# Performance work log

Measured on AMD Instinct MI355X. Metric: run time of the kernel, lower is better.

## Reference

```python
import jax, jax.numpy as jnp
import numpy as np

DT = 1.0  # LEM base time-step


def _conv(x, w, b):
    # x: [B,C,H,W], w: [O,I,kh,kw] 'SAME' stride-1 conv (kernel=3, padding=1)
    y = jax.lax.conv_general_dilated(
        x, w, window_strides=(1, 1), padding='SAME',
        dimension_numbers=('NCHW', 'OIHW', 'NCHW'))
    return y + b[None, :, None, None]


def setup_inputs() -> dict:
    key = jax.random.key(0)
    ks = jax.random.split(key, 7)
    B, Cin, Cout, T, H, W, K = 8, 32, 32, 50, 64, 64, 3
    s = 0.1
    return {
        'X':  jax.random.normal(ks[0], (B, Cin, T, H, W), jnp.float32),
        'Wx': jax.random.normal(ks[1], (4 * Cout, Cin, K, K), jnp.float32) * s,
        'bx': jnp.zeros((4 * Cout,), jnp.float32),
        'Wy': jax.random.normal(ks[2], (3 * Cout, Cout, K, K), jnp.float32) * s,
        'by': jnp.zeros((3 * Cout,), jnp.float32),
        'Wz': jax.random.normal(ks[3], (Cout, Cout, K, K), jnp.float32) * s,
        'bz': jnp.zeros((Cout,), jnp.float32),
    }


def reference(X, Wx, bx, Wy, by, Wz, bz):
    B, Cin, T, H, W = X.shape
    Cout = Wz.shape[0]

    def step(carry, x_t):
        Y, Z = carry
        # gates/candidates from input and hidden state
        xg1, xg2, xz, xy = jnp.split(_conv(x_t, Wx, bx), 4, axis=1)
        yg1, yg2, yz = jnp.split(_conv(Y, Wy, by), 3, axis=1)
        ms1 = DT * jax.nn.sigmoid(xg1 + yg1)  # dt-bar gate
        ms2 = DT * jax.nn.sigmoid(xg2 + yg2)  # dt-hat gate
        Z_new = (1.0 - ms1) * Z + ms1 * jnp.tanh(xz + yz)
        Y_new = (1.0 - ms2) * Y + ms2 * jnp.tanh(xy + _conv(Z_new, Wz, bz))
        return (Y_new, Z_new), Y_new

    Y0 = jnp.zeros((B, Cout, H, W), X.dtype)
    Z0 = jnp.zeros((B, Cout, H, W), X.dtype)
    xs = jnp.moveaxis(X, 2, 0)  # [T,B,Cin,H,W]
    _, ys = jax.lax.scan(step, (Y0, Z0), xs)
    return jnp.moveaxis(ys, 0, 2)  # [B,Cout,T,H,W]
```

## Files before the change

### kernel.cpp

```cpp
#include <hip/hip_runtime.h>
#include <math.h>

#define HH 64
#define WW 64
#define NB 8
#define CIN 32
#define COUT 32
#define NT 50
#define HW (HH*WW)
#define CSX ((size_t)NT*HW)
#define PITCH 20

__device__ __forceinline__ float fsigmoid(float x) {
    return 1.0f / (1.0f + __expf(-x));
}
__device__ __forceinline__ float ftanh(float x) {
    float e = __expf(-2.0f * fabsf(x));
    float t = (1.0f - e) / (1.0f + e);
    return copysignf(t, x);
}

__global__ __launch_bounds__(256) void wtrans(
    const float* __restrict__ Wx, const float* __restrict__ Wy, const float* __restrict__ Wz,
    float* __restrict__ Wxt, float* __restrict__ Wyt, float* __restrict__ Wzt)
{
    int i = blockIdx.x * 256 + threadIdx.x;
    if (i < 36864) {
        int g = (i >> 2) & 3, o = i & 3;
        int q = i >> 4;
        int cg = q & 7, t2 = q >> 3;
        int ci = t2 & 31, k = t2 >> 5;
        int oc = g*32 + cg*4 + o;
        Wxt[i] = Wx[((size_t)oc*32 + ci)*9 + k];
    }
    if (i < 27648) {
        int r12 = i % 12, q = i / 12;
        int g = r12 >> 2, o = r12 & 3;
        int cg = q & 7, t2 = q >> 3;
        int ci = t2 & 31, k = t2 >> 5;
        int oc = g*32 + cg*4 + o;
        Wyt[i] = Wy[((size_t)oc*32 + ci)*9 + k];
    }
    if (i < 9216) {
        int o = i & 3, q = i >> 2;
        int cg = q & 7, t2 = q >> 3;
        int ci = t2 & 31, k = t2 >> 5;
        int oc = cg*4 + o;
        Wzt[i] = Wz[((size_t)oc*32 + ci)*9 + k];
    }
}

__device__ __forceinline__ void stage16(float* tile,
    const float* __restrict__ src, size_t cstride, int h0, int w0, int tid)
{
    #pragma unroll
    for (int it = 0; it < 3; ++it) {
        int idx = it*512 + tid;
        if (idx < 1296) {
            int ci4 = idx / 324;
            int pix = idx - ci4*324;
            int rr = pix / 18, cc = pix - rr*18;
            int gh = h0 + rr - 1, gw = w0 + cc - 1;
            int inb = (int)((unsigned)gh < 64u) & (int)((unsigned)gw < 64u);
            int ghc = min(max(gh, 0), HH-1), gwc = min(max(gw, 0), WW-1);
            const float* p = src + (size_t)(ci4*4)*cstride + (ghc*WW + gwc);
            float a0 = p[0];
            float a1 = p[cstride];
            float a2 = p[2*cstride];
            float a3 = p[3*cstride];
            float4 q;
            q.x = inb ? a0 : 0.0f;
            q.y = inb ? a1 : 0.0f;
            q.z = inb ? a2 : 0.0f;
            q.w = inb ? a3 : 0.0f;
            *(float4*)&tile[pix*PITCH + ci4*4] = q;
        }
    }
}

__global__ __launch_bounds__(512, 4) void lem_gates(
    const float* __restrict__ X,
    const float* __restrict__ Wxt, const float* __restrict__ bx,
    const float* __restrict__ Wyt, const float* __restrict__ by,
    const float* __restrict__ Y, float* __restrict__ Z,
    float* __restrict__ ms2w, float* __restrict__ xyw, int t)
{
    __shared__ __align__(16) float tile[324*PITCH];
    const int tid = threadIdx.x;
    const int tx = tid & 15, ty = (tid >> 4) & 15;
    const int half = __builtin_amdgcn_readfirstlane(tid >> 8);
    const int w0 = blockIdx.x * 16, h0 = blockIdx.y * 16;
    const int b  = blockIdx.z >> 2;
    const int cg = ((blockIdx.z & 3) << 1) | half;

    float ax[16], ay[12];
    #pragma unroll
    for (int i = 0; i < 16; i++) ax[i] = 0.0f;
    #pragma unroll
    for (int i = 0; i < 12; i++) ay[i] = 0.0f;

    const float* xb = X + ((size_t)b*CIN*NT + t)*HW;
    #pragma unroll
    for (int c = 0; c < 2; ++c) {
        stage16(tile, xb + (size_t)(c*16)*CSX, CSX, h0, w0, tid);
        __syncthreads();
        for (int k = 0; k < 9; ++k) {
            int kh = k/3, kw = k - kh*3;
            const float* lp = &tile[((ty+kh)*18 + tx+kw)*PITCH];
            const float* wp = Wxt + ((size_t)((k*32 + c*16)*8) + cg)*16;
            #pragma unroll
            for (int ci4 = 0; ci4 < 4; ++ci4) {
                float4 xv = *(const float4*)(lp + ci4*4);
                #pragma unroll
                for (int j = 0; j < 4; ++j) {
                    float v = (j==0)?xv.x:(j==1)?xv.y:(j==2)?xv.z:xv.w;
                    const float4* wr = (const float4*)(wp + (size_t)(ci4*4+j)*128);
                    #pragma unroll
                    for (int g = 0; g < 4; ++g) {
                        float4 wg = wr[g];
                        ax[g*4+0] = fmaf(v, wg.x, ax[g*4+0]);
                        ax[g*4+1] = fmaf(v, wg.y, ax[g*4+1]);
                        ax[g*4+2] = fmaf(v, wg.z, ax[g*4+2]);
                        ax[g*4+3] = fmaf(v, wg.w, ax[g*4+3]);
                    }
                }
            }
        }
        __syncthreads();
    }

    const float* yb = Y + (size_t)b*COUT*HW;
    #pragma unroll
    for (int c = 0; c < 2; ++c) {
        stage16(tile, yb + (size_t)(c*16)*HW, (size_t)HW, h0, w0, tid);
        __syncthreads();
        for (int k = 0; k < 9; ++k) {
            int kh = k/3, kw = k - kh*3;
            const float* lp = &tile[((ty+kh)*18 + tx+kw)*PITCH];
            const float* wp = Wyt + ((size_t)((k*32 + c*16)*8) + cg)*12;
            #pragma unroll
            for (int ci4 = 0; ci4 < 4; ++ci4) {
                float4 xv = *(const float4*)(lp + ci4*4);
                #pragma unroll
                for (int j = 0; j < 4; ++j) {
                    float v = (j==0)?xv.x:(j==1)?xv.y:(j==2)?xv.z:xv.w;
                    const float4* wr = (const float4*)(wp + (size_t)(ci4*4+j)*96);
                    #pragma unroll
                    for (int g = 0; g < 3; ++g) {
                        float4 wg = wr[g];
                        ay[g*4+0] = fmaf(v, wg.x, ay[g*4+0]);
                        ay[g*4+1] = fmaf(v, wg.y, ay[g*4+1]);
                        ay[g*4+2] = fmaf(v, wg.z, ay[g*4+2]);
                        ay[g*4+3] = fmaf(v, wg.w, ay[g*4+3]);
                    }
                }
            }
        }
        __syncthreads();
    }

    const int h = h0 + ty, w = w0 + tx;
    #pragma unroll
    for (int ch = 0; ch < 4; ++ch) {
        int c = cg*4 + ch;
        size_t si = ((size_t)(b*COUT + c))*HW + h*WW + w;
        float g1 = ax[0+ch]  + bx[c]        + ay[0+ch] + by[c];
        float g2 = ax[4+ch]  + bx[COUT+c]   + ay[4+ch] + by[COUT+c];
        float zc = ax[8+ch]  + bx[2*COUT+c] + ay[8+ch] + by[2*COUT+c];
        float xy = ax[12+ch] + bx[3*COUT+c];
        float m1 = fsigmoid(g1);
        float zn = (1.0f - m1) * Z[si] + m1 * ftanh(zc);
        Z[si]    = zn;
        ms2w[si] = fsigmoid(g2);
        xyw[si]  = xy;
    }
}

__global__ __launch_bounds__(512, 4) void lem_update(
    const float* __restrict__ Wzt, const float* __restrict__ bz,
    const float* __restrict__ Z, float* __restrict__ Y,
    const float* __restrict__ ms2w, const float* __restrict__ xyw,
    float* __restrict__ out, int t)
{
    __shared__ __align__(16) float tile[324*PITCH];
    const int tid = threadIdx.x;
    const int tx = tid & 15, ty = (tid >> 4) & 15;
    const int half = __builtin_amdgcn_readfirstlane(tid >> 8);
    const int w0 = blockIdx.x * 16, h0 = blockIdx.y * 16;
    const int b  = blockIdx.z >> 2;
    const int cg = ((blockIdx.z & 3) << 1) | half;

    float az[4] = {0.f, 0.f, 0.f, 0.f};

    const float* zb = Z + (size_t)b*COUT*HW;
    #pragma unroll
    for (int c = 0; c < 2; ++c) {
        stage16(tile, zb + (size_t)(c*16)*HW, (size_t)HW, h0, w0, tid);
        __syncthreads();
        for (int k = 0; k < 9; ++k) {
            int kh = k/3, kw = k - kh*3;
            const float* lp = &tile[((ty+kh)*18 + tx+kw)*PITCH];
            const float* wp = Wzt + ((size_t)((k*32 + c*16)*8) + cg)*4;
            #pragma unroll
            for (int ci4 = 0; ci4 < 4; ++ci4) {
                float4 xv = *(const float4*)(lp + ci4*4);
                #pragma unroll
                for (int j = 0; j < 4; ++j) {
                    float v = (j==0)?xv.x:(j==1)?xv.y:(j==2)?xv.z:xv.w;
                    float4 wg = *(const float4*)(wp + (size_t)(ci4*4+j)*32);
                    az[0] = fmaf(v, wg.x, az[0]);
                    az[1] = fmaf(v, wg.y, az[1]);
                    az[2] = fmaf(v, wg.z, az[2]);
                    az[3] = fmaf(v, wg.w, az[3]);
                }
            }
        }
        __syncthreads();
    }

    const int h = h0 + ty, w = w0 + tx;
    #pragma unroll
    for (int ch = 0; ch < 4; ++ch) {
        int c = cg*4 + ch;
        size_t si = ((size_t)(b*COUT + c))*HW + h*WW + w;
        float m2 = ms2w[si];
        float yn = (1.0f - m2) * Y[si] + m2 * ftanh(xyw[si] + az[ch] + bz[c]);
        Y[si] = yn;
        out[((size_t)(b*COUT + c)*NT + t)*HW + h*WW + w] = yn;
    }
}

extern "C" void kernel_launch(void* const* d_in, const int* in_sizes, int n_in,
                              void* d_out, int out_size, void* d_ws, size_t ws_size,
                              hipStream_t stream)
{
    const float* X  = (const float*)d_in[0];
    const float* Wx = (const float*)d_in[1];
    const float* bx = (const float*)d_in[2];
    const float* Wy = (const float*)d_in[3];
    const float* by = (const float*)d_in[4];
    const float* Wz = (const float*)d_in[5];
    const float* bz = (const float*)d_in[6];
    float* out = (float*)d_out;
    float* ws  = (float*)d_ws;

    const size_t S = (size_t)NB*COUT*HW;
    float* Y   = ws;
    float* Z   = ws + S;
    float* m2w = ws + 2*S;
    float* xyw = ws + 3*S;
    float* Wxt = ws + 4*S;
    float* Wyt = Wxt + 36864;
    float* Wzt = Wyt + 27648;

    hipMemsetAsync(Y, 0, 2*S*sizeof(float), stream);
    wtrans<<<dim3(144), dim3(256), 0, stream>>>(Wx, Wy, Wz, Wxt, Wyt, Wzt);

    dim3 grid(WW/16, HH/16, NB*4);
    for (int t = 0; t < NT; t++) {
        lem_gates <<<grid, 512, 0, stream>>>(X, Wxt, bx, Wyt, by, Y, Z, m2w, xyw, t);
        lem_update<<<grid, 512, 0, stream>>>(Wzt, bz, Z, Y, m2w, xyw, out, t);
    }
}
```

Baseline: 6.303 ms.

## Double-buffer LDS tiles and prefetch next chunk into registers during convolution

Splits tile staging into a global-load issue phase and an LDS write phase, and double-buffers the shared-memory tile. The next channel chunk is loaded into registers while the current chunk is convolved, which removes one barrier per chunk and hides global latency. Epilogue operands (old Z/Y, ms2, xy, biases) are also loaded up front. Doubling LDS (about 52KB per block) and holding more registers may reduce occupancy below the 4 blocks per CU requested by launch bounds.

```diff
diff --git a/kernel.cpp b/kernel.cpp
--- a/kernel.cpp
+++ b/kernel.cpp
@@ -10,6 +10,7 @@
 #define HW (HH*WW)
 #define CSX ((size_t)NT*HW)
 #define PITCH 20
+#define TSZ (324*PITCH)
 
 __device__ __forceinline__ float fsigmoid(float x) {
     return 1.0f / (1.0f + __expf(-x));
@@ -50,30 +51,75 @@
     }
 }
 
-__device__ __forceinline__ void stage16(float* tile,
+struct StageRegs {
+    float4 v[3];
+    int    dst[3];
+    int    inb[3];
+};
+
+__device__ __forceinline__ void stage_issue(StageRegs& s,
     const float* __restrict__ src, size_t cstride, int h0, int w0, int tid)
 {
     #pragma unroll
     for (int it = 0; it < 3; ++it) {
         int idx = it*512 + tid;
+        s.dst[it] = -1;
         if (idx < 1296) {
             int ci4 = idx / 324;
             int pix = idx - ci4*324;
             int rr = pix / 18, cc = pix - rr*18;
             int gh = h0 + rr - 1, gw = w0 + cc - 1;
-            int inb = (int)((unsigned)gh < 64u) & (int)((unsigned)gw < 64u);
+            s.inb[it] = (int)((unsigned)gh < 64u) & (int)((unsigned)gw < 64u);
             int ghc = min(max(gh, 0), HH-1), gwc = min(max(gw, 0), WW-1);
             const float* p = src + (size_t)(ci4*4)*cstride + (ghc*WW + gwc);
-            float a0 = p[0];
-            float a1 = p[cstride];
-            float a2 = p[2*cstride];
-            float a3 = p[3*cstride];
+            s.v[it].x = p[0];
+            s.v[it].y = p[cstride];
+            s.v[it].z = p[2*cstride];
+            s.v[it].w = p[3*cstride];
+            s.dst[it] = pix*PITCH + ci4*4;
+        }
+    }
+}
+
+__device__ __forceinline__ void stage_write(float* __restrict__ buf, const StageRegs& s)
+{
+    #pragma unroll
+    for (int it = 0; it < 3; ++it) {
+        if (s.dst[it] >= 0) {
             float4 q;
-            q.x = inb ? a0 : 0.0f;
-            q.y = inb ? a1 : 0.0f;
-            q.z = inb ? a2 : 0.0f;
-            q.w = inb ? a3 : 0.0f;
-            *(float4*)&tile[pix*PITCH + ci4*4] = q;
+            q.x = s.inb[it] ? s.v[it].x : 0.0f;
+            q.y = s.inb[it] ? s.v[it].y : 0.0f;
+            q.z = s.inb[it] ? s.v[it].z : 0.0f;
+            q.w = s.inb[it] ? s.v[it].w : 0.0f;
+            *(float4*)&buf[s.dst[it]] = q;
+        }
+    }
+}
+
+template<int NG>
+__device__ __forceinline__ void conv_chunk(const float* __restrict__ buf,
+    const float* __restrict__ wbase, int ty, int tx, float* __restrict__ acc)
+{
+    for (int k = 0; k < 9; ++k) {
+        int kh = k/3, kw = k - kh*3;
+        const float* lp = &buf[((ty+kh)*18 + tx+kw)*PITCH];
+        const float* wp = wbase + (size_t)k*(32*8*NG*4);
+        #pragma unroll
+        for (int ci4 = 0; ci4 < 4; ++ci4) {
+            float4 xv = *(const float4*)(lp + ci4*4);
+            #pragma unroll
+            for (int j = 0; j < 4; ++j) {
+                float v = (j==0)?xv.x:(j==1)?xv.y:(j==2)?xv.z:xv.w;
+                const float4* wr = (const float4*)(wp + (size_t)(ci4*4+j)*(8*NG*4));
+                #pragma unroll
+                for (int g = 0; g < NG; ++g) {
+                    float4 wg = wr[g];
+                    acc[g*4+0] = fmaf(v, wg.x, acc[g*4+0]);
+                    acc[g*4+1] = fmaf(v, wg.y, acc[g*4+1]);
+                    acc[g*4+2] = fmaf(v, wg.z, acc[g*4+2]);
+                    acc[g*4+3] = fmaf(v, wg.w, acc[g*4+3]);
+                }
+            }
         }
     }
 }
@@ -85,7 +131,7 @@
     const float* __restrict__ Y, float* __restrict__ Z,
     float* __restrict__ ms2w, float* __restrict__ xyw, int t)
 {
-    __shared__ __align__(16) float tile[324*PITCH];
+    __shared__ __align__(16) float tile[2][TSZ];
     const int tid = threadIdx.x;
     const int tx = tid & 15, ty = (tid >> 4) & 15;
     const int half = __builtin_amdgcn_readfirstlane(tid >> 8);
@@ -93,83 +139,62 @@
     const int b  = blockIdx.z >> 2;
     const int cg = ((blockIdx.z & 3) << 1) | half;
 
+    const float* xb = X + ((size_t)b*CIN*NT + t)*HW;
+    const float* yb = Y + (size_t)b*COUT*HW;
+
+    const int h = h0 + ty, w = w0 + tx;
+    const size_t si0 = ((size_t)(b*COUT + cg*4))*HW + h*WW + w;
+    float zold[4];
+    #pragma unroll
+    for (int ch = 0; ch < 4; ++ch) zold[ch] = Z[si0 + (size_t)ch*HW];
+    float bxr[16], byr[12];
+    #pragma unroll
+    for (int g = 0; g < 4; ++g)
+        #pragma unroll
+        for (int ch = 0; ch < 4; ++ch) bxr[g*4+ch] = bx[g*32 + cg*4 + ch];
+    #pragma unroll
+    for (int g = 0; g < 3; ++g)
+        #pragma unroll
+        for (int ch = 0; ch < 4; ++ch) byr[g*4+ch] = by[g*32 + cg*4 + ch];
+
     float ax[16], ay[12];
     #pragma unroll
     for (int i = 0; i < 16; i++) ax[i] = 0.0f;
     #pragma unroll
     for (int i = 0; i < 12; i++) ay[i] = 0.0f;
 
-    const float* xb = X + ((size_t)b*CIN*NT + t)*HW;
-    #pragma unroll
-    for (int c = 0; c < 2; ++c) {
-        stage16(tile, xb + (size_t)(c*16)*CSX, CSX, h0, w0, tid);
-        __syncthreads();
-        for (int k = 0; k < 9; ++k) {
-            int kh = k/3, kw = k - kh*3;
-            const float* lp = &tile[((ty+kh)*18 + tx+kw)*PITCH];
-            const float* wp = Wxt + ((size_t)((k*32 + c*16)*8) + cg)*16;
-            #pragma unroll
-            for (int ci4 = 0; ci4 < 4; ++ci4) {
-                float4 xv = *(const float4*)(lp + ci4*4);
-                #pragma unroll
-                for (int j = 0; j < 4; ++j) {
-                    float v = (j==0)?xv.x:(j==1)?xv.y:(j==2)?xv.z:xv.w;
-                    const float4* wr = (const float4*)(wp + (size_t)(ci4*4+j)*128);
-                    #pragma unroll
-                    for (int g = 0; g < 4; ++g) {
-                        float4 wg = wr[g];
-                        ax[g*4+0] = fmaf(v, wg.x, ax[g*4+0]);
-                        ax[g*4+1] = fmaf(v, wg.y, ax[g*4+1]);
-                        ax[g*4+2] = fmaf(v, wg.z, ax[g*4+2]);
-                        ax[g*4+3] = fmaf(v, wg.w, ax[g*4+3]);
-                    }
-                }
-            }
-        }
-        __syncthreads();
-    }
-
-    const float* yb = Y + (size_t)b*COUT*HW;
-    #pragma unroll
-    for (int c = 0; c < 2; ++c) {
-        stage16(tile, yb + (size_t)(c*16)*HW, (size_t)HW, h0, w0, tid);
-        __syncthreads();
-        for (int k = 0; k < 9; ++k) {
-            int kh = k/3, kw = k - kh*3;
-            const float* lp = &tile[((ty+kh)*18 + tx+kw)*PITCH];
-            const float* wp = Wyt + ((size_t)((k*32 + c*16)*8) + cg)*12;
-            #pragma unroll
-            for (int ci4 = 0; ci4 < 4; ++ci4) {
-                float4 xv = *(const float4*)(lp + ci4*4);
-                #pragma unroll
-                for (int j = 0; j < 4; ++j) {
-                    float v = (j==0)?xv.x:(j==1)?xv.y:(j==2)?xv.z:xv.w;
-                    const float4* wr = (const float4*)(wp + (size_t)(ci4*4+j)*96);
-                    #pragma unroll
-                    for (int g = 0; g < 3; ++g) {
-                        float4 wg = wr[g];
-                        ay[g*4+0] = fmaf(v, wg.x, ay[g*4+0]);
-                        ay[g*4+1] = fmaf(v, wg.y, ay[g*4+1]);
-                        ay[g*4+2] = fmaf(v, wg.z, ay[g*4+2]);
-                        ay[g*4+3] = fmaf(v, wg.w, ay[g*4+3]);
-                    }
-                }
-            }
-        }
-        __syncthreads();
-    }
-
-    const int h = h0 + ty, w = w0 + tx;
+    StageRegs sr;
+
+    stage_issue(sr, xb, CSX, h0, w0, tid);
+    stage_write(tile[0], sr);
+    __syncthreads();
+
+    stage_issue(sr, xb + (size_t)16*CSX, CSX, h0, w0, tid);
+    conv_chunk<4>(tile[0], Wxt + ((size_t)(0*16*8) + cg)*16, ty, tx, ax);
+    stage_write(tile[1], sr);
+    __syncthreads();
+
+    stage_issue(sr, yb, (size_t)HW, h0, w0, tid);
+    conv_chunk<4>(tile[1], Wxt + ((size_t)(1*16*8) + cg)*16, ty, tx, ax);
+    stage_write(tile[0], sr);
+    __syncthreads();
+
+    stage_issue(sr, yb + (size_t)16*HW, (size_t)HW, h0, w0, tid);
+    conv_chunk<3>(tile[0], Wyt + ((size_t)(0*16*8) + cg)*12, ty, tx, ay);
+    stage_write(tile[1], sr);
+    __syncthreads();
+
+    conv_chunk<3>(tile[1], Wyt + ((size_t)(1*16*8) + cg)*12, ty, tx, ay);
+
     #pragma unroll
     for (int ch = 0; ch < 4; ++ch) {
-        int c = cg*4 + ch;
-        size_t si = ((size_t)(b*COUT + c))*HW + h*WW + w;
-        float g1 = ax[0+ch]  + bx[c]        + ay[0+ch] + by[c];
-        float g2 = ax[4+ch]  + bx[COUT+c]   + ay[4+ch] + by[COUT+c];
-        float zc = ax[8+ch]  + bx[2*COUT+c] + ay[8+ch] + by[2*COUT+c];
-        float xy = ax[12+ch] + bx[3*COUT+c];
+        size_t si = si0 + (size_t)ch*HW;
+        float g1 = ax[0+ch]  + bxr[0+ch]  + ay[0+ch] + byr[0+ch];
+        float g2 = ax[4+ch]  + bxr[4+ch]  + ay[4+ch] + byr[4+ch];
+        float zc = ax[8+ch]  + bxr[8+ch]  + ay[8+ch] + byr[8+ch];
+        float xy = ax[12+ch] + bxr[12+ch];
         float m1 = fsigmoid(g1);
-        float zn = (1.0f - m1) * Z[si] + m1 * ftanh(zc);
+        float zn = (1.0f - m1) * zold[ch] + m1 * ftanh(zc);
         Z[si]    = zn;
         ms2w[si] = fsigmoid(g2);
         xyw[si]  = xy;
@@ -182,7 +207,7 @@
     const float* __restrict__ ms2w, const float* __restrict__ xyw,
     float* __restrict__ out, int t)
 {
-    __shared__ __align__(16) float tile[324*PITCH];
+    __shared__ __align__(16) float tile[2][TSZ];
     const int tid = threadIdx.x;
     const int tx = tid & 15, ty = (tid >> 4) & 15;
     const int half = __builtin_amdgcn_readfirstlane(tid >> 8);
@@ -190,43 +215,40 @@
     const int b  = blockIdx.z >> 2;
     const int cg = ((blockIdx.z & 3) << 1) | half;
 
+    const float* zb = Z + (size_t)b*COUT*HW;
+
+    const int h = h0 + ty, w = w0 + tx;
+    const size_t si0 = ((size_t)(b*COUT + cg*4))*HW + h*WW + w;
+    float m2r[4], xyr[4], yold[4], bzr[4];
+    #pragma unroll
+    for (int ch = 0; ch < 4; ++ch) {
+        m2r[ch] = ms2w[si0 + (size_t)ch*HW];
+        xyr[ch] = xyw[si0 + (size_t)ch*HW];
+        yold[ch] = Y[si0 + (size_t)ch*HW];
+        bzr[ch] = bz[cg*4 + ch];
+    }
+
     float az[4] = {0.f, 0.f, 0.f, 0.f};
-
-    const float* zb = Z + (size_t)b*COUT*HW;
-    #pragma unroll
-    for (int c = 0; c < 2; ++c) {
-        stage16(tile, zb + (size_t)(c*16)*HW, (size_t)HW, h0, w0, tid);
-        __syncthreads();
-        for (int k = 0; k < 9; ++k) {
-            int kh = k/3, kw = k - kh*3;
-            const float* lp = &tile[((ty+kh)*18 + tx+kw)*PITCH];
-            const float* wp = Wzt + ((size_t)((k*32 + c*16)*8) + cg)*4;
-            #pragma unroll
-            for (int ci4 = 0; ci4 < 4; ++ci4) {
-                float4 xv = *(const float4*)(lp + ci4*4);
-                #pragma unroll
-                for (int j = 0; j < 4; ++j) {
-                    float v = (j==0)?xv.x:(j==1)?xv.y:(j==2)?xv.z:xv.w;
-                    float4 wg = *(const float4*)(wp + (size_t)(ci4*4+j)*32);
-                    az[0] = fmaf(v, wg.x, az[0]);
-                    az[1] = fmaf(v, wg.y, az[1]);
-                    az[2] = fmaf(v, wg.z, az[2]);
-                    az[3] = fmaf(v, wg.w, az[3]);
-                }
-            }
-        }
-        __syncthreads();
-    }
-
-    const int h = h0 + ty, w = w0 + tx;
+    StageRegs sr;
+
+    stage_issue(sr, zb, (size_t)HW, h0, w0, tid);
+    stage_write(tile[0], sr);
+    __syncthreads();
+
+    stage_issue(sr, zb + (size_t)16*HW, (size_t)HW, h0, w0, tid);
+    conv_chunk<1>(tile[0], Wzt + ((size_t)(0*16*8) + cg)*4, ty, tx, az);
+    stage_write(tile[1], sr);
+    __syncthreads();
+
+    conv_chunk<1>(tile[1], Wzt + ((size_t)(1*16*8) + cg)*4, ty, tx, az);
+
     #pragma unroll
     for (int ch = 0; ch < 4; ++ch) {
-        int c = cg*4 + ch;
-        size_t si = ((size_t)(b*COUT + c))*HW + h*WW + w;
-        float m2 = ms2w[si];
-        float yn = (1.0f - m2) * Y[si] + m2 * ftanh(xyw[si] + az[ch] + bz[c]);
+        size_t si = si0 + (size_t)ch*HW;
+        float m2 = m2r[ch];
+        float yn = (1.0f - m2) * yold[ch] + m2 * ftanh(xyr[ch] + az[ch] + bzr[ch]);
         Y[si] = yn;
-        out[((size_t)(b*COUT + c)*NT + t)*HW + h*WW + w] = yn;
+        out[((size_t)(b*COUT + cg*4 + ch)*NT + t)*HW + h*WW + w] = yn;
     }
 }
 
```

Result: slower. 6.577 ms (+4.3%).
